# Kernel optimization log

Hardware: AMD Instinct MI355X
Metric: run time of the kernel (lower is better)

## Reference

```python
import jax, jax.numpy as jnp
import numpy as np

CAPACITY = 0.7
TEMP = 0.5          # initial_temp, never annealed (global_step=None path)
LB_WEIGHT = 0.005
Z_WEIGHT = 5e-06
EPS = 1e-10


def setup_inputs() -> dict:
    key = jax.random.key(0)
    k1, k2, k3 = jax.random.split(key, 3)
    B, S, H = 4, 8192, 2048
    return {
        "hidden_states": jax.random.normal(k1, (B, S, H), dtype=jnp.float32),
        "active_mask": jnp.ones((B, S), dtype=bool),
        "u": jax.random.uniform(k2, (B, S), dtype=jnp.float32),
        # router: nn.Linear(H, 1), weight ~ N(0, 0.02), bias = 0
        "w": jax.random.normal(k3, (H,), dtype=jnp.float32) * 0.02,
        "b": jnp.zeros((), dtype=jnp.float32),
    }


def reference(hidden_states, active_mask, u, w, b):
    B, S = active_mask.shape
    N = B * S
    # mask is all-True by construction -> num_active = N, k static
    num_active = N
    k = max(1, min(int(CAPACITY * num_active), num_active))

    # scores = router(hidden).squeeze(-1)  -> [B,S]
    scores = jnp.einsum("bsh,h->bs", hidden_states, w) + b
    scores = jnp.where(active_mask, scores, -jnp.inf)

    # gumbel noise from uniform u (matches torch.rand_like path)
    gumbel = -jnp.log(-jnp.log(u + EPS) + EPS)
    noisy = ((scores + gumbel) / TEMP).reshape(-1)  # [N]

    _, idx = jax.lax.top_k(noisy, k)
    ffn_mask = jnp.zeros((N,), dtype=bool).at[idx].set(True)
    ffn_mask = ffn_mask.reshape(B, S) & active_mask

    # aux losses (masked reductions over active tokens)
    maskf = active_mask.astype(jnp.float32)
    na = maskf.sum()
    safe_scores = jnp.where(active_mask, scores, 0.0)
    f = ffn_mask.astype(jnp.float32).sum() / na
    p = (jax.nn.sigmoid(safe_scores) * maskf).sum() / na
    lb_loss = (f - CAPACITY) ** 2 + (p - CAPACITY) ** 2
    z_loss = (safe_scores ** 2 * maskf).sum() / na
    aux_loss = LB_WEIGHT * lb_loss + Z_WEIGHT * z_loss

    return ffn_mask, aux_loss
```

## Files before the change

kernel.cpp:

```cpp
#include <hip/hip_runtime.h>
#include <math.h>

#define NTOK 32768
#define HDIM 2048
#define K_SEL 22937
#define EPS_F 1e-10f
#define SBLK 1024

__global__ __launch_bounds__(256) void score_kernel(
    const float* __restrict__ hidden,
    const float* __restrict__ u,
    const float* __restrict__ w,
    const float* __restrict__ b,
    unsigned int* __restrict__ keys,
    float* __restrict__ pp,
    float* __restrict__ zz)
{
    const int wave = threadIdx.x >> 6;
    const int lane = threadIdx.x & 63;
    const int row0 = blockIdx.x * 32 + wave * 8;

    const float4* __restrict__ w4 = (const float4*)w;
    float4 wr[8];
    #pragma unroll
    for (int j = 0; j < 8; ++j) wr[j] = w4[j * 64 + lane];

    const float4* __restrict__ rowp = (const float4*)(hidden + (size_t)row0 * HDIM);

    float sums[8];
    float4 buf[2][8];
    #pragma unroll
    for (int j = 0; j < 8; ++j) buf[0][j] = rowp[j * 64 + lane];

    #pragma unroll
    for (int r = 0; r < 8; ++r) {
        const int cur = r & 1, nxt = cur ^ 1;
        if (r < 7) {
            #pragma unroll
            for (int j = 0; j < 8; ++j)
                buf[nxt][j] = rowp[(r + 1) * 512 + j * 64 + lane];
        }
        float s = 0.0f;
        #pragma unroll
        for (int j = 0; j < 8; ++j) {
            const float4 hv = buf[cur][j];
            s += hv.x * wr[j].x + hv.y * wr[j].y + hv.z * wr[j].z + hv.w * wr[j].w;
        }
        sums[r] = s;
    }

    #pragma unroll
    for (int off = 32; off > 0; off >>= 1) {
        #pragma unroll
        for (int r = 0; r < 8; ++r)
            sums[r] += __shfl_down(sums[r], off, 64);
    }

    __shared__ float red_p[4], red_z[4];
    if (lane == 0) {
        const float bias = b[0];
        float p_acc = 0.0f, z_acc = 0.0f;
        #pragma unroll
        for (int r = 0; r < 8; ++r) {
            const float score = sums[r] + bias;
            const float uu = u[row0 + r];
            const float g = -logf(-logf(uu + EPS_F) + EPS_F);
            const float noisy = (score + g) * 2.0f;
            const unsigned int bits = __float_as_uint(noisy);
            keys[row0 + r] = (bits & 0x80000000u) ? ~bits : (bits | 0x80000000u);
            p_acc += 1.0f / (1.0f + expf(-score));
            z_acc += score * score;
        }
        red_p[wave] = p_acc;
        red_z[wave] = z_acc;
    }
    __syncthreads();
    if (threadIdx.x == 0) {
        pp[blockIdx.x] = red_p[0] + red_p[1] + red_p[2] + red_p[3];
        zz[blockIdx.x] = red_z[0] + red_z[1] + red_z[2] + red_z[3];
    }
}

#define HSHIFT 19
#define HBINS  (1 << (32 - HSHIFT))

__global__ __launch_bounds__(1024) void tau_kernel(
    const unsigned int* __restrict__ keys,
    const float* __restrict__ pp,
    const float* __restrict__ zz,
    unsigned int* __restrict__ meta,
    float* __restrict__ out)
{
    __shared__ unsigned int shist[HBINS];
    __shared__ unsigned int wcnt[16];
    __shared__ int sB;
    __shared__ float wredp[16], wredz[16];

    const int t = threadIdx.x;
    const int lane = t & 63;
    const int wid = t >> 6;

    #pragma unroll
    for (int i = 0; i < HBINS / 1024; ++i) shist[t * (HBINS / 1024) + i] = 0u;

    uint4 k4[8];
    const uint4* kk4 = (const uint4*)keys;
    #pragma unroll
    for (int j = 0; j < 8; ++j) k4[j] = kk4[1024 * j + t];
    unsigned int myk[32];
    #pragma unroll
    for (int j = 0; j < 8; ++j) {
        myk[4 * j + 0] = k4[j].x;
        myk[4 * j + 1] = k4[j].y;
        myk[4 * j + 2] = k4[j].z;
        myk[4 * j + 3] = k4[j].w;
    }
    __syncthreads();

    #pragma unroll
    for (int m = 0; m < 32; ++m) atomicAdd(&shist[myk[m] >> HSHIFT], 1u);
    __syncthreads();

    {
        const int g = HBINS / 1024;
        unsigned int s = 0;
        #pragma unroll
        for (int i = 0; i < g; ++i) s += shist[t * g + i];
        unsigned int suf = s;
        #pragma unroll
        for (int off = 1; off < 64; off <<= 1) {
            const unsigned int n = __shfl_down(suf, off, 64);
            if (lane + off < 64) suf += n;
        }
        if (lane == 0) wcnt[wid] = suf;
        __syncthreads();
        unsigned int hi = 0;
        for (int i = wid + 1; i < 16; ++i) hi += wcnt[i];
        const unsigned int SufT = suf + hi;
        if (SufT >= (unsigned int)K_SEL && SufT - s < (unsigned int)K_SEL) {
            unsigned int run = SufT - s;
            for (int bb = g - 1; bb >= 0; --bb) {
                run += shist[t * g + bb];
                if (run >= (unsigned int)K_SEL) { sB = t * g + bb; break; }
            }
        }
        __syncthreads();
    }
    unsigned int tau = ((unsigned int)sB) << HSHIFT;

    auto blocksum = [&](unsigned int c) -> unsigned int {
        #pragma unroll
        for (int off = 32; off > 0; off >>= 1) c += __shfl_down(c, off, 64);
        if (lane == 0) wcnt[wid] = c;
        __syncthreads();
        unsigned int tot = 0;
        #pragma unroll
        for (int i = 0; i < 16; ++i) tot += wcnt[i];
        __syncthreads();
        return tot;
    };

    for (int bit = HSHIFT - 1; bit >= 0; --bit) {
        const unsigned int cand = tau | (1u << bit);
        unsigned int c = 0;
        #pragma unroll
        for (int m = 0; m < 32; ++m) c += (myk[m] >= cand) ? 1u : 0u;
        if (blocksum(c) >= (unsigned int)K_SEL) tau = cand;
    }

    unsigned int cgt = 0, ceq = 0;
    #pragma unroll
    for (int m = 0; m < 32; ++m) {
        cgt += (myk[m] > tau) ? 1u : 0u;
        ceq += (myk[m] == tau) ? 1u : 0u;
    }
    const unsigned int totp = blocksum((cgt << 16) | ceq);
    const unsigned int tot_gt = totp >> 16;
    const unsigned int tot_eq = totp & 0xFFFFu;
    const unsigned int needed = (unsigned int)K_SEL - tot_gt;

    unsigned int X = NTOK - 1;
    if (needed < tot_eq) {
        auto cntle = [&](unsigned int cand) -> unsigned int {
            unsigned int c = 0;
            #pragma unroll
            for (int m = 0; m < 32; ++m) {
                const unsigned int idx = 4096u * (m >> 2) + 4u * t + (m & 3);
                c += (myk[m] == tau && idx <= cand) ? 1u : 0u;
            }
            return blocksum(c);
        };
        if (cntle(0) >= needed) {
            X = 0;
        } else {
            unsigned int Y = 0;
            for (int bit = 14; bit >= 0; --bit) {
                const unsigned int cand = Y | (1u << bit);
                if (cntle(cand) < needed) Y = cand;
            }
            X = Y + 1;
        }
    }

    if (t == 0) { meta[0] = tau; meta[1] = X; }

    float lp = pp[t], lz = zz[t];
    #pragma unroll
    for (int off = 32; off > 0; off >>= 1) {
        lp += __shfl_down(lp, off, 64);
        lz += __shfl_down(lz, off, 64);
    }
    if (lane == 0) { wredp[wid] = lp; wredz[wid] = lz; }
    __syncthreads();
    if (t == 0) {
        float sp = 0.0f, sz = 0.0f;
        for (int i = 0; i < 16; ++i) { sp += wredp[i]; sz += wredz[i]; }
        const float na = (float)NTOK;
        const float f = (float)K_SEL / na;
        const float p = sp / na;
        const float z = sz / na;
        const float d1 = f - 0.7f;
        const float d2 = p - 0.7f;
        out[NTOK] = 0.005f * (d1 * d1 + d2 * d2) + 5e-6f * z;
    }
}

__global__ __launch_bounds__(128) void mask_kernel(
    const unsigned int* __restrict__ keys,
    const unsigned int* __restrict__ meta,
    float* __restrict__ out)
{
    const unsigned int tau = meta[0];
    const unsigned int X = meta[1];
    const int i = blockIdx.x * 128 + threadIdx.x;
    const uint4 kv = ((const uint4*)keys)[i];
    const unsigned int e = 4u * (unsigned int)i;
    float4 o;
    o.x = (kv.x > tau || (kv.x == tau && e     <= X)) ? 1.0f : 0.0f;
    o.y = (kv.y > tau || (kv.y == tau && e + 1 <= X)) ? 1.0f : 0.0f;
    o.z = (kv.z > tau || (kv.z == tau && e + 2 <= X)) ? 1.0f : 0.0f;
    o.w = (kv.w > tau || (kv.w == tau && e + 3 <= X)) ? 1.0f : 0.0f;
    ((float4*)out)[i] = o;
}

extern "C" void kernel_launch(void* const* d_in, const int* in_sizes, int n_in,
                              void* d_out, int out_size, void* d_ws, size_t ws_size,
                              hipStream_t stream) {
    const float* hidden = (const float*)d_in[0];
    const float* u = (const float*)d_in[2];
    const float* w = (const float*)d_in[3];
    const float* b = (const float*)d_in[4];
    float* out = (float*)d_out;

    const size_t KEYS_B = (size_t)NTOK * sizeof(unsigned int);
    const size_t PART_B = (size_t)SBLK * sizeof(float);
    const size_t META_B = 256;

    char* wsp = (char*)d_ws;
    unsigned int *keys, *meta;
    float *pp, *zz;

    if (ws_size >= KEYS_B + 2 * PART_B + META_B) {
        keys = (unsigned int*)wsp;
        pp = (float*)(wsp + KEYS_B);
        zz = pp + SBLK;
        meta = (unsigned int*)(wsp + KEYS_B + 2 * PART_B);
    } else {
        keys = (unsigned int*)d_out;
        pp = (float*)wsp;
        zz = pp + SBLK;
        meta = (unsigned int*)(wsp + 2 * PART_B);
    }

    score_kernel<<<SBLK, 256, 0, stream>>>(hidden, u, w, b, keys, pp, zz);
    tau_kernel<<<1, 1024, 0, stream>>>(keys, pp, zz, meta, out);
    mask_kernel<<<64, 128, 0, stream>>>(keys, meta, out);
}
```

Measured before the change: 394.6 us.

## Use two-level radix histogram for threshold and fuse mask write into tau kernel

Replaces 19 bit-by-bit block-wide count reductions with a second shared-memory histogram pass over the next 13 bits, leaving only 6 bisection steps. The separate mask kernel is removed: the single-block tau kernel writes the output mask directly from the keys it holds in registers, so one launch and the meta round trip go away. The cost is a second atomic histogram pass and serialising the mask stores onto one block. In the fallback path where keys alias the output buffer, every thread reads its keys into registers before any stores, so that should remain safe.

Measured after the change: 384.1 us. 2.7% less time.

```diff
diff --git a/kernel.cpp b/kernel.cpp
--- a/kernel.cpp
+++ b/kernel.cpp
@@ -83,12 +83,12 @@
 
 #define HSHIFT 19
 #define HBINS  (1 << (32 - HSHIFT))
+#define HSHIFT2 6
 
 __global__ __launch_bounds__(1024) void tau_kernel(
     const unsigned int* __restrict__ keys,
     const float* __restrict__ pp,
     const float* __restrict__ zz,
-    unsigned int* __restrict__ meta,
     float* __restrict__ out)
 {
     __shared__ unsigned int shist[HBINS];
@@ -99,9 +99,10 @@
     const int t = threadIdx.x;
     const int lane = t & 63;
     const int wid = t >> 6;
-
-    #pragma unroll
-    for (int i = 0; i < HBINS / 1024; ++i) shist[t * (HBINS / 1024) + i] = 0u;
+    const int g = HBINS / 1024;
+
+    #pragma unroll
+    for (int i = 0; i < g; ++i) shist[t * g + i] = 0u;
 
     uint4 k4[8];
     const uint4* kk4 = (const uint4*)keys;
@@ -121,8 +122,7 @@
     for (int m = 0; m < 32; ++m) atomicAdd(&shist[myk[m] >> HSHIFT], 1u);
     __syncthreads();
 
-    {
-        const int g = HBINS / 1024;
+    auto histscan = [&](unsigned int Kth) -> unsigned int {
         unsigned int s = 0;
         #pragma unroll
         for (int i = 0; i < g; ++i) s += shist[t * g + i];
@@ -137,16 +137,16 @@
         unsigned int hi = 0;
         for (int i = wid + 1; i < 16; ++i) hi += wcnt[i];
         const unsigned int SufT = suf + hi;
-        if (SufT >= (unsigned int)K_SEL && SufT - s < (unsigned int)K_SEL) {
+        if (SufT >= Kth && SufT - s < Kth) {
             unsigned int run = SufT - s;
             for (int bb = g - 1; bb >= 0; --bb) {
                 run += shist[t * g + bb];
-                if (run >= (unsigned int)K_SEL) { sB = t * g + bb; break; }
+                if (run >= Kth) { sB = t * g + bb; break; }
             }
         }
         __syncthreads();
-    }
-    unsigned int tau = ((unsigned int)sB) << HSHIFT;
+        return (unsigned int)sB;
+    };
 
     auto blocksum = [&](unsigned int c) -> unsigned int {
         #pragma unroll
@@ -160,7 +160,27 @@
         return tot;
     };
 
-    for (int bit = HSHIFT - 1; bit >= 0; --bit) {
+    const unsigned int B1 = histscan((unsigned int)K_SEL);
+    unsigned int tau = B1 << HSHIFT;
+
+    unsigned int ca = 0;
+    #pragma unroll
+    for (int m = 0; m < 32; ++m) ca += ((myk[m] >> HSHIFT) > B1) ? 1u : 0u;
+    const unsigned int cnt_above = blocksum(ca);
+    const unsigned int K2 = (unsigned int)K_SEL - cnt_above;
+
+    #pragma unroll
+    for (int i = 0; i < g; ++i) shist[t * g + i] = 0u;
+    __syncthreads();
+    #pragma unroll
+    for (int m = 0; m < 32; ++m)
+        if ((myk[m] >> HSHIFT) == B1)
+            atomicAdd(&shist[(myk[m] >> HSHIFT2) & (HBINS - 1)], 1u);
+    __syncthreads();
+    const unsigned int B2 = histscan(K2);
+    tau |= B2 << HSHIFT2;
+
+    for (int bit = HSHIFT2 - 1; bit >= 0; --bit) {
         const unsigned int cand = tau | (1u << bit);
         unsigned int c = 0;
         #pragma unroll
@@ -202,7 +222,20 @@
         }
     }
 
-    if (t == 0) { meta[0] = tau; meta[1] = X; }
+    #pragma unroll
+    for (int j = 0; j < 8; ++j) {
+        const unsigned int e = 4096u * (unsigned int)j + 4u * (unsigned int)t;
+        const unsigned int a0 = myk[4 * j + 0];
+        const unsigned int a1 = myk[4 * j + 1];
+        const unsigned int a2 = myk[4 * j + 2];
+        const unsigned int a3 = myk[4 * j + 3];
+        float4 o;
+        o.x = (a0 > tau || (a0 == tau && e     <= X)) ? 1.0f : 0.0f;
+        o.y = (a1 > tau || (a1 == tau && e + 1 <= X)) ? 1.0f : 0.0f;
+        o.z = (a2 > tau || (a2 == tau && e + 2 <= X)) ? 1.0f : 0.0f;
+        o.w = (a3 > tau || (a3 == tau && e + 3 <= X)) ? 1.0f : 0.0f;
+        ((float4*)out)[1024 * j + t] = o;
+    }
 
     float lp = pp[t], lz = zz[t];
     #pragma unroll
@@ -225,24 +258,6 @@
     }
 }
 
-__global__ __launch_bounds__(128) void mask_kernel(
-    const unsigned int* __restrict__ keys,
-    const unsigned int* __restrict__ meta,
-    float* __restrict__ out)
-{
-    const unsigned int tau = meta[0];
-    const unsigned int X = meta[1];
-    const int i = blockIdx.x * 128 + threadIdx.x;
-    const uint4 kv = ((const uint4*)keys)[i];
-    const unsigned int e = 4u * (unsigned int)i;
-    float4 o;
-    o.x = (kv.x > tau || (kv.x == tau && e     <= X)) ? 1.0f : 0.0f;
-    o.y = (kv.y > tau || (kv.y == tau && e + 1 <= X)) ? 1.0f : 0.0f;
-    o.z = (kv.z > tau || (kv.z == tau && e + 2 <= X)) ? 1.0f : 0.0f;
-    o.w = (kv.w > tau || (kv.w == tau && e + 3 <= X)) ? 1.0f : 0.0f;
-    ((float4*)out)[i] = o;
-}
-
 extern "C" void kernel_launch(void* const* d_in, const int* in_sizes, int n_in,
                               void* d_out, int out_size, void* d_ws, size_t ws_size,
                               hipStream_t stream) {
@@ -254,25 +269,21 @@
 
     const size_t KEYS_B = (size_t)NTOK * sizeof(unsigned int);
     const size_t PART_B = (size_t)SBLK * sizeof(float);
-    const size_t META_B = 256;
 
     char* wsp = (char*)d_ws;
-    unsigned int *keys, *meta;
+    unsigned int* keys;
     float *pp, *zz;
 
-    if (ws_size >= KEYS_B + 2 * PART_B + META_B) {
+    if (ws_size >= KEYS_B + 2 * PART_B) {
         keys = (unsigned int*)wsp;
         pp = (float*)(wsp + KEYS_B);
         zz = pp + SBLK;
-        meta = (unsigned int*)(wsp + KEYS_B + 2 * PART_B);
     } else {
         keys = (unsigned int*)d_out;
         pp = (float*)wsp;
         zz = pp + SBLK;
-        meta = (unsigned int*)(wsp + 2 * PART_B);
     }
 
     score_kernel<<<SBLK, 256, 0, stream>>>(hidden, u, w, b, keys, pp, zz);
-    tau_kernel<<<1, 1024, 0, stream>>>(keys, pp, zz, meta, out);
-    mask_kernel<<<64, 128, 0, stream>>>(keys, meta, out);
+    tau_kernel<<<1, 1024, 0, stream>>>(keys, pp, zz, out);
 }
```
